# Kernel tuning notes

Measured on AMD Instinct MI355X. Metric: run time of the kernel, lower is better.

Reference implementation:

```python
import jax, jax.numpy as jnp
import numpy as np

N_NODES = 50000
N_EDGES = 600000
N_REL = 64
D = 128
N_LAYERS = 2


def setup_inputs() -> dict:
    key = jax.random.key(0)
    k1, k2, k3, k4, k5, k6 = jax.random.split(key, 6)
    return {
        "entity_table": jax.random.normal(k1, (N_NODES, D), jnp.float32) * 0.05,
        "relation_table": jax.random.normal(k2, (N_REL, D), jnp.float32) * 0.05,
        "W": jax.random.normal(k3, (N_LAYERS, 2 * D, D), jnp.float32) * 0.05,
        "b": jnp.zeros((N_LAYERS, D), jnp.float32),
        "edge_dst": jax.random.randint(k4, (N_EDGES,), 0, N_NODES),
        "edge_nbr": jax.random.randint(k5, (N_EDGES,), 0, N_NODES),
        "edge_rel": jax.random.randint(k6, (N_EDGES,), 0, N_REL),
    }


def _segment_softmax(score, seg, num_segments):
    # numerically stable per-destination-node softmax over incoming edges
    smax = jax.ops.segment_max(score, seg, num_segments=num_segments)
    ex = jnp.exp(score - smax[seg])
    denom = jax.ops.segment_sum(ex, seg, num_segments=num_segments)
    return ex / denom[seg]


def reference(entity_table, relation_table, W, b, edge_dst, edge_nbr, edge_rel):
    n_nodes, d = entity_table.shape
    n_layers = W.shape[0]
    deg = jax.ops.segment_sum(jnp.ones_like(edge_dst, dtype=entity_table.dtype),
                              edge_dst, num_segments=n_nodes)
    has_nbr = (deg > 0)[:, None]  # [N,1]

    # relation-attentive query uses the BASE entity embedding of the dst node
    # (the torch code passes entity_embedder(current_node) each layer)
    q = jnp.tanh(entity_table[edge_dst] + relation_table[edge_rel])  # [E,d]

    prev = entity_table
    for l in range(n_layers):
        nbr_emb = prev[edge_nbr]                      # [E,d] gather
        score = jnp.sum(nbr_emb * q, axis=-1)         # [E]
        alpha = _segment_softmax(score, edge_dst, n_nodes)
        neigh = jax.ops.segment_sum(alpha[:, None] * nbr_emb, edge_dst,
                                    num_segments=n_nodes)  # [N,d]
        h = jnp.concatenate([prev, neigh], axis=-1) @ W[l] + b[l]
        h = jax.nn.leaky_relu(h)                      # LeakyReLU slope 0.01
        h = h / jnp.linalg.norm(h, axis=-1, keepdims=True)
        # nodes with no neighbours keep their base entity embedding
        prev = jnp.where(has_nbr, h, entity_table)
    return prev
```

## Files before the change

kernel.cpp:

```cpp
#include <hip/hip_runtime.h>
#include <math.h>

#define NN 50000
#define NE 600000
#define NR 64
#define DD 128
#define FB 586
#define DEGS 16

typedef __attribute__((ext_vector_type(2))) _Float16 h2;
typedef __attribute__((ext_vector_type(4))) _Float16 h4;
typedef __attribute__((ext_vector_type(8))) _Float16 h8;
typedef __attribute__((ext_vector_type(4))) float f32x4;


__device__ __forceinline__ h2 tanh_h2(h2 x) {
    const h2 C5 = {(_Float16)0.1333333333f,  (_Float16)0.1333333333f};
    const h2 C3 = {(_Float16)-0.3333333333f, (_Float16)-0.3333333333f};
    const h2 ONE = {(_Float16)1.f, (_Float16)1.f};
    h2 x2 = x * x;
    h2 p = x2 * C5 + C3;
    p = x2 * p + ONE;
    return x * p;
}

template <int CTRL, int ROW_MASK>
__device__ __forceinline__ float dpp_add(float x) {
    int xi = __builtin_bit_cast(int, x);
    int yi = __builtin_amdgcn_update_dpp(0, xi, CTRL, ROW_MASK, 0xF, true);
    return x + __builtin_bit_cast(float, yi);
}


__global__ __launch_bounds__(256) void prep_k(const float* __restrict__ ent,
                                              const float* __restrict__ rel,
                                              const float* __restrict__ W,
                                              const int* __restrict__ edst,
                                              const int* __restrict__ enbr,
                                              const int* __restrict__ erel,
                                              _Float16* __restrict__ Ah,
                                              _Float16* __restrict__ relh,
                                              _Float16* __restrict__ wp,
                                              int* __restrict__ deg,
                                              int* __restrict__ bucket) {
    int b = blockIdx.x;
    if (b < FB) {
        int e = (b * 256 + threadIdx.x) * 4;
        if (e < NE) {
            int4 d  = *(const int4*)&edst[e];
            int4 nb = *(const int4*)&enbr[e];
            int4 rl = *(const int4*)&erel[e];
            int r0 = atomicAdd(&deg[d.x * DEGS], 1);
            int r1 = atomicAdd(&deg[d.y * DEGS], 1);
            int r2 = atomicAdd(&deg[d.z * DEGS], 1);
            int r3 = atomicAdd(&deg[d.w * DEGS], 1);
            if (r0 < 64) bucket[d.x * 64 + r0] = nb.x | (rl.x << 16);
            if (r1 < 64) bucket[d.y * 64 + r1] = nb.y | (rl.y << 16);
            if (r2 < 64) bucket[d.z * 64 + r2] = nb.z | (rl.z << 16);
            if (r3 < 64) bucket[d.w * 64 + r3] = nb.w | (rl.w << 16);
        }
    } else if (b < FB + 6250) {
        int tid = (b - FB) * 256 + threadIdx.x;
        int node = tid >> 5, c = tid & 31;
        float4 v = *(const float4*)&ent[(size_t)node * DD + c * 4];
        h4 o = {(_Float16)v.x, (_Float16)v.y, (_Float16)v.z, (_Float16)v.w};
        *(h4*)&Ah[(size_t)node * 256 + c * 4] = o;
    } else if (b < FB + 6258) {
        int tid = (b - FB - 6250) * 256 + threadIdx.x;
        float4 v = *(const float4*)&rel[tid * 4];
        h4 o = {(_Float16)v.x, (_Float16)v.y, (_Float16)v.z, (_Float16)v.w};
        *(h4*)&relh[tid * 4] = o;
    } else {
        int tid = (b - FB - 6258) * 256 + threadIdx.x;
        int lane = tid & 63;
        int ct   = (tid >> 6) & 7;
        int ks   = (tid >> 9) & 7;
        int l    = tid >> 12;
        int q = lane >> 4, n = lane & 15;
        const float* Wl = W + (size_t)l * 256 * 128;
        _Float16* dst = wp + ((((size_t)l * 8 + ks) * 8 + ct) * 64 + lane) * 8;
#pragma unroll
        for (int j = 0; j < 8; ++j) {
            int k = ks * 32 + q * 8 + j;
            dst[j] = (_Float16)Wl[(size_t)k * 128 + ct * 16 + n];
        }
    }
}


__global__ __launch_bounds__(256) void agg_k(const _Float16* __restrict__ Ah,
                                             const _Float16* __restrict__ Aq,
                                             const _Float16* __restrict__ relh,
                                             const int* __restrict__ deg_,
                                             const int* __restrict__ bucket,
                                             _Float16* __restrict__ Ah_out) {
    int lane = threadIdx.x & 63;
    int grp  = lane >> 4;
    int t16  = lane & 15;
    int wid  = threadIdx.x >> 6;
    int node = blockIdx.x * 4 + wid;
    int dg = deg_[node * DEGS];

    unsigned dof = (unsigned)t16 * 8u;
    h8 qv = *(const h8*)&Aq[(unsigned)node * 256u + dof];
    h2 q0 = {qv[0], qv[1]}, q1 = {qv[2], qv[3]}, q2 = {qv[4], qv[5]}, q3 = {qv[6], qv[7]};

    float l = 0.f;
    h2 acc0 = {(_Float16)0.f, (_Float16)0.f};
    h2 acc1 = acc0, acc2 = acc0, acc3 = acc0;

    if (dg > 0) {
        int e0 = node * 64;
        int e1 = e0 + dg;
        int iters = (dg + 3) >> 2;
        int last = e1 - 1;
        int ei = e0 + grp;

        int pk_c = bucket[min(ei, last)];
        h8 nb_c = *(const h8*)&Ah[(unsigned)(pk_c & 0xFFFF) * 256u + dof];
        h8 rl_c = *(const h8*)&relh[(unsigned)(pk_c >> 16) * 128u + dof];
        int pk_n = bucket[min(ei + 4, last)];

#pragma unroll 2
        for (int it = 0; it < iters; ++it) {
            int pk_n2 = bucket[min(ei + 8, last)];
            h8 nb_n = *(const h8*)&Ah[(unsigned)(pk_n & 0xFFFF) * 256u + dof];
            h8 rl_n = *(const h8*)&relh[(unsigned)(pk_n >> 16) * 128u + dof];

            h2 n0 = {nb_c[0], nb_c[1]}, n1 = {nb_c[2], nb_c[3]};
            h2 n2 = {nb_c[4], nb_c[5]}, n3 = {nb_c[6], nb_c[7]};
            h2 r0 = {rl_c[0], rl_c[1]}, r1 = {rl_c[2], rl_c[3]};
            h2 r2 = {rl_c[4], rl_c[5]}, r3 = {rl_c[6], rl_c[7]};

            h2 sd = n0 * tanh_h2(q0 + r0);
            sd = n1 * tanh_h2(q1 + r1) + sd;
            sd = n2 * tanh_h2(q2 + r2) + sd;
            sd = n3 * tanh_h2(q3 + r3) + sd;
            float s = (float)sd.x + (float)sd.y;

            s = dpp_add<0x111, 0xF>(s);
            s = dpp_add<0x112, 0xF>(s);
            s = dpp_add<0x114, 0xF>(s);
            s = dpp_add<0x118, 0xF>(s);
            int si = __builtin_amdgcn_ds_swizzle(__builtin_bit_cast(int, s), 0x1F0);
            s = __builtin_bit_cast(float, si);

            float p = (ei < e1) ? __expf(s) : 0.f;
            l += p;
            _Float16 ph = (_Float16)p;
            h2 p2 = {ph, ph};
            acc0 = p2 * n0 + acc0;
            acc1 = p2 * n1 + acc1;
            acc2 = p2 * n2 + acc2;
            acc3 = p2 * n3 + acc3;

            ei += 4;
            pk_c = pk_n; pk_n = pk_n2;
            nb_c = nb_n; rl_c = rl_n;
        }

#pragma unroll
        for (int off = 16; off <= 32; off <<= 1) {
            acc0 += __builtin_bit_cast(h2, __shfl_xor(__builtin_bit_cast(int, acc0), off, 64));
            acc1 += __builtin_bit_cast(h2, __shfl_xor(__builtin_bit_cast(int, acc1), off, 64));
            acc2 += __builtin_bit_cast(h2, __shfl_xor(__builtin_bit_cast(int, acc2), off, 64));
            acc3 += __builtin_bit_cast(h2, __shfl_xor(__builtin_bit_cast(int, acc3), off, 64));
            l += __shfl_xor(l, off, 64);
        }
    }

    float inv = (dg > 0) ? __builtin_amdgcn_rcpf(l) : 0.f;
    if (grp == 0) {
        _Float16 ih = (_Float16)inv;
        h2 iv = {ih, ih};
        h2 o0 = acc0 * iv, o1 = acc1 * iv, o2 = acc2 * iv, o3 = acc3 * iv;
        h8 o = {o0.x, o0.y, o1.x, o1.y, o2.x, o2.y, o3.x, o3.y};
        *(h8*)&Ah_out[(unsigned)node * 256u + 128u + dof] = o;
    }
}


template <bool LAST>
__global__ __launch_bounds__(256) void upd_k(const _Float16* __restrict__ Ah,
                                             const _Float16* __restrict__ wp,
                                             const float* __restrict__ bl,
                                             const int* __restrict__ deg_,
                                             const float* __restrict__ ent,
                                             float* __restrict__ out,
                                             _Float16* __restrict__ Ahn) {
    int lane = threadIdx.x & 63, wid = threadIdx.x >> 6;
    int quad = lane >> 4, n16 = lane & 15;
    int row0 = (blockIdx.x * 4 + wid) * 16;
    int arow = min(row0 + n16, NN - 1);

    f32x4 acc[8];
#pragma unroll
    for (int ct = 0; ct < 8; ++ct) acc[ct] = (f32x4){0.f, 0.f, 0.f, 0.f};

    const h8* aptr = (const h8*)(Ah + (size_t)arow * 256 + quad * 8);
#pragma unroll
    for (int ks = 0; ks < 8; ++ks) {
        h8 af = aptr[ks * 4];
        const h8* bp = (const h8*)(wp + (((size_t)ks * 8) * 64 + lane) * 8);
#pragma unroll
        for (int ct = 0; ct < 8; ++ct) {
            h8 bfrag = bp[ct * 64];
            acc[ct] = __builtin_amdgcn_mfma_f32_16x16x32_f16(af, bfrag, acc[ct], 0, 0, 0);
        }
    }

    float bias[8];
#pragma unroll
    for (int ct = 0; ct < 8; ++ct) bias[ct] = bl[ct * 16 + n16];

#pragma unroll
    for (int r = 0; r < 4; ++r) {
        int orow = row0 + quad * 4 + r;
        float h[8];
        float ss = 0.f;
#pragma unroll
        for (int ct = 0; ct < 8; ++ct) {
            float v = acc[ct][r] + bias[ct];
            v = (v > 0.f) ? v : 0.01f * v;
            h[ct] = v;
            ss += v * v;
        }
        ss = dpp_add<0x111, 0xF>(ss);
        ss = dpp_add<0x112, 0xF>(ss);
        ss = dpp_add<0x114, 0xF>(ss);
        ss = dpp_add<0x118, 0xF>(ss);
        ss = __shfl(ss, 15, 16);
        float rinv = rsqrtf(ss);

        if (orow < NN) {
            bool iso = deg_[orow * DEGS] == 0;
#pragma unroll
            for (int ct = 0; ct < 8; ++ct) {
                int col = ct * 16 + n16;
                float v = h[ct] * rinv;
                if (iso) v = ent[(size_t)orow * DD + col];
                if (LAST) out[(size_t)orow * DD + col] = v;
                else      Ahn[(size_t)orow * 256 + col] = (_Float16)v;
            }
        }
    }
}


extern "C" void kernel_launch(void* const* d_in, const int* in_sizes, int n_in,
                              void* d_out, int out_size, void* d_ws, size_t ws_size,
                              hipStream_t stream) {
    const float* ent = (const float*)d_in[0];
    const float* rel = (const float*)d_in[1];
    const float* W   = (const float*)d_in[2];
    const float* b   = (const float*)d_in[3];
    const int* edst  = (const int*)d_in[4];
    const int* enbr  = (const int*)d_in[5];
    const int* erel  = (const int*)d_in[6];
    float* out = (float*)d_out;

    char* ws = (char*)d_ws;
    size_t off = 0;
    auto alloc = [&](size_t bytes) -> void* {
        void* p = ws + off;
        off += (bytes + 255) & ~(size_t)255;
        return p;
    };
    int* deg       = (int*)alloc((size_t)NN * DEGS * 4);
    int* bucket    = (int*)alloc((size_t)NN * 64 * 4);
    _Float16* Ah0  = (_Float16*)alloc((size_t)NN * 256 * 2);
    _Float16* Ah1  = (_Float16*)alloc((size_t)NN * 256 * 2);
    _Float16* wp   = (_Float16*)alloc((size_t)2 * 8 * 8 * 64 * 8 * 2);
    _Float16* relh = (_Float16*)alloc((size_t)NR * DD * 2);

    hipMemsetAsync(deg, 0, (size_t)NN * DEGS * 4, stream);
    prep_k<<<FB + 6290, 256, 0, stream>>>(ent, rel, W, edst, enbr, erel,
                                          Ah0, relh, wp, deg, bucket);

    const _Float16* wp0 = wp;
    const _Float16* wp1 = wp + (size_t)8 * 8 * 64 * 8;
    int ublocks = (NN + 63) / 64;

    agg_k<<<NN / 4, 256, 0, stream>>>(Ah0, Ah0, relh, deg, bucket, Ah0);
    upd_k<false><<<ublocks, 256, 0, stream>>>(Ah0, wp0, b, deg, ent, out, Ah1);

    agg_k<<<NN / 4, 256, 0, stream>>>(Ah1, Ah0, relh, deg, bucket, Ah1);
    upd_k<true><<<ublocks, 256, 0, stream>>>(Ah1, wp1, b + DD, deg, ent, out, Ah0);
}
```

Measured before the change: 221.9 us.

## Compact layer-1 embedding buffer, drop gather clamps, stage update output through LDS

Layer-1 node embeddings now go into a dense 128-wide fp16 buffer instead of the first half of a 256-wide one. This halves the row stride the second aggregation gathers from and reuses Ah0's aggregation slot. The per-edge min() against the segment end is replaced by clamping the neighbour index and masking the relation id, with the bucket buffer padded so reads past the segment stay in bounds. The update kernel writes its results into a shared-memory tile and then stores whole rows with 16-byte vector writes, reading the isolated-node check once per row. The cost is extra LDS use and a __syncthreads in the update kernel.

Result: faster. 213.2 us (-3.9%).

```diff
diff --git a/kernel.cpp b/kernel.cpp
--- a/kernel.cpp
+++ b/kernel.cpp
@@ -7,6 +7,7 @@
 #define DD 128
 #define FB 586
 #define DEGS 16
+#define TS 134
 
 typedef __attribute__((ext_vector_type(2))) _Float16 h2;
 typedef __attribute__((ext_vector_type(4))) _Float16 h4;
@@ -88,12 +89,13 @@
 }
 
 
-__global__ __launch_bounds__(256) void agg_k(const _Float16* __restrict__ Ah,
+template <int NBS>
+__global__ __launch_bounds__(256) void agg_k(const _Float16* __restrict__ nbuf,
                                              const _Float16* __restrict__ Aq,
                                              const _Float16* __restrict__ relh,
                                              const int* __restrict__ deg_,
                                              const int* __restrict__ bucket,
-                                             _Float16* __restrict__ Ah_out) {
+                                             _Float16* __restrict__ aggout) {
     int lane = threadIdx.x & 63;
     int grp  = lane >> 4;
     int t16  = lane & 15;
@@ -113,19 +115,20 @@
         int e0 = node * 64;
         int e1 = e0 + dg;
         int iters = (dg + 3) >> 2;
-        int last = e1 - 1;
         int ei = e0 + grp;
 
-        int pk_c = bucket[min(ei, last)];
-        h8 nb_c = *(const h8*)&Ah[(unsigned)(pk_c & 0xFFFF) * 256u + dof];
-        h8 rl_c = *(const h8*)&relh[(unsigned)(pk_c >> 16) * 128u + dof];
-        int pk_n = bucket[min(ei + 4, last)];
+        int pk_c = bucket[ei];
+        unsigned ni_c = min((unsigned)(pk_c & 0xFFFF), (unsigned)(NN - 1));
+        h8 nb_c = *(const h8*)&nbuf[ni_c * (unsigned)NBS + dof];
+        h8 rl_c = *(const h8*)&relh[(unsigned)((pk_c >> 16) & 63) * 128u + dof];
+        int pk_n = bucket[ei + 4];
 
 #pragma unroll 2
         for (int it = 0; it < iters; ++it) {
-            int pk_n2 = bucket[min(ei + 8, last)];
-            h8 nb_n = *(const h8*)&Ah[(unsigned)(pk_n & 0xFFFF) * 256u + dof];
-            h8 rl_n = *(const h8*)&relh[(unsigned)(pk_n >> 16) * 128u + dof];
+            int pk_n2 = bucket[ei + 8];
+            unsigned ni_n = min((unsigned)(pk_n & 0xFFFF), (unsigned)(NN - 1));
+            h8 nb_n = *(const h8*)&nbuf[ni_n * (unsigned)NBS + dof];
+            h8 rl_n = *(const h8*)&relh[(unsigned)((pk_n >> 16) & 63) * 128u + dof];
 
             h2 n0 = {nb_c[0], nb_c[1]}, n1 = {nb_c[2], nb_c[3]};
             h2 n2 = {nb_c[4], nb_c[5]}, n3 = {nb_c[6], nb_c[7]};
@@ -175,19 +178,24 @@
         h2 iv = {ih, ih};
         h2 o0 = acc0 * iv, o1 = acc1 * iv, o2 = acc2 * iv, o3 = acc3 * iv;
         h8 o = {o0.x, o0.y, o1.x, o1.y, o2.x, o2.y, o3.x, o3.y};
-        *(h8*)&Ah_out[(unsigned)node * 256u + 128u + dof] = o;
-    }
-}
-
-
-template <bool LAST>
-__global__ __launch_bounds__(256) void upd_k(const _Float16* __restrict__ Ah,
+        *(h8*)&aggout[(unsigned)node * 256u + 128u + dof] = o;
+    }
+}
+
+
+template <bool LAST, int SP>
+__global__ __launch_bounds__(256) void upd_k(const _Float16* __restrict__ prev,
+                                             const _Float16* __restrict__ agg,
                                              const _Float16* __restrict__ wp,
                                              const float* __restrict__ bl,
                                              const int* __restrict__ deg_,
                                              const float* __restrict__ ent,
                                              float* __restrict__ out,
                                              _Float16* __restrict__ Ahn) {
+    __shared__ __align__(16) char ltile[64 * TS * 4];
+    float    (*t32)[TS] = (float(*)[TS])ltile;
+    _Float16 (*t16)[TS] = (_Float16(*)[TS])ltile;
+
     int lane = threadIdx.x & 63, wid = threadIdx.x >> 6;
     int quad = lane >> 4, n16 = lane & 15;
     int row0 = (blockIdx.x * 4 + wid) * 16;
@@ -197,10 +205,11 @@
 #pragma unroll
     for (int ct = 0; ct < 8; ++ct) acc[ct] = (f32x4){0.f, 0.f, 0.f, 0.f};
 
-    const h8* aptr = (const h8*)(Ah + (size_t)arow * 256 + quad * 8);
+    const h8* apP = (const h8*)(prev + (size_t)arow * SP + quad * 8);
+    const h8* apQ = (const h8*)(agg + (size_t)arow * 256 + 128 + quad * 8);
 #pragma unroll
     for (int ks = 0; ks < 8; ++ks) {
-        h8 af = aptr[ks * 4];
+        h8 af = (ks < 4) ? apP[ks * 4] : apQ[(ks - 4) * 4];
         const h8* bp = (const h8*)(wp + (((size_t)ks * 8) * 64 + lane) * 8);
 #pragma unroll
         for (int ct = 0; ct < 8; ++ct) {
@@ -215,7 +224,7 @@
 
 #pragma unroll
     for (int r = 0; r < 4; ++r) {
-        int orow = row0 + quad * 4 + r;
+        int lrow = wid * 16 + quad * 4 + r;
         float h[8];
         float ss = 0.f;
 #pragma unroll
@@ -232,15 +241,49 @@
         ss = __shfl(ss, 15, 16);
         float rinv = rsqrtf(ss);
 
-        if (orow < NN) {
-            bool iso = deg_[orow * DEGS] == 0;
-#pragma unroll
-            for (int ct = 0; ct < 8; ++ct) {
-                int col = ct * 16 + n16;
-                float v = h[ct] * rinv;
-                if (iso) v = ent[(size_t)orow * DD + col];
-                if (LAST) out[(size_t)orow * DD + col] = v;
-                else      Ahn[(size_t)orow * 256 + col] = (_Float16)v;
+#pragma unroll
+        for (int ct = 0; ct < 8; ++ct) {
+            int col = ct * 16 + n16;
+            float v = h[ct] * rinv;
+            if (LAST) t32[lrow][col] = v;
+            else      t16[lrow][col] = (_Float16)v;
+        }
+    }
+
+    __syncthreads();
+
+    int t = threadIdx.x;
+    int lrow = t >> 2, q = t & 3;
+    int grow = blockIdx.x * 64 + lrow;
+    if (grow < NN) {
+        bool iso = deg_[grow * DEGS] == 0;
+        const float* erow = ent + (size_t)grow * DD + q * 32;
+        if (!LAST) {
+            _Float16* dst = Ahn + (size_t)grow * 128 + q * 32;
+            if (!iso) {
+#pragma unroll
+                for (int k = 0; k < 4; ++k)
+                    *(h8*)&dst[k * 8] = *(const h8*)&t16[lrow][q * 32 + k * 8];
+            } else {
+#pragma unroll
+                for (int k = 0; k < 4; ++k) {
+                    float4 a = *(const float4*)&erow[k * 8];
+                    float4 c = *(const float4*)&erow[k * 8 + 4];
+                    h8 o = {(_Float16)a.x, (_Float16)a.y, (_Float16)a.z, (_Float16)a.w,
+                            (_Float16)c.x, (_Float16)c.y, (_Float16)c.z, (_Float16)c.w};
+                    *(h8*)&dst[k * 8] = o;
+                }
+            }
+        } else {
+            float* dst = out + (size_t)grow * DD + q * 32;
+            if (!iso) {
+#pragma unroll
+                for (int k = 0; k < 8; ++k)
+                    *(float4*)&dst[k * 4] = *(const float4*)&t32[lrow][q * 32 + k * 4];
+            } else {
+#pragma unroll
+                for (int k = 0; k < 8; ++k)
+                    *(float4*)&dst[k * 4] = *(const float4*)&erow[k * 4];
             }
         }
     }
@@ -267,9 +310,9 @@
         return p;
     };
     int* deg       = (int*)alloc((size_t)NN * DEGS * 4);
-    int* bucket    = (int*)alloc((size_t)NN * 64 * 4);
+    int* bucket    = (int*)alloc((size_t)NN * 64 * 4 + 256);
     _Float16* Ah0  = (_Float16*)alloc((size_t)NN * 256 * 2);
-    _Float16* Ah1  = (_Float16*)alloc((size_t)NN * 256 * 2);
+    _Float16* Ah1  = (_Float16*)alloc((size_t)NN * 128 * 2);
     _Float16* wp   = (_Float16*)alloc((size_t)2 * 8 * 8 * 64 * 8 * 2);
     _Float16* relh = (_Float16*)alloc((size_t)NR * DD * 2);
 
@@ -281,9 +324,9 @@
     const _Float16* wp1 = wp + (size_t)8 * 8 * 64 * 8;
     int ublocks = (NN + 63) / 64;
 
-    agg_k<<<NN / 4, 256, 0, stream>>>(Ah0, Ah0, relh, deg, bucket, Ah0);
-    upd_k<false><<<ublocks, 256, 0, stream>>>(Ah0, wp0, b, deg, ent, out, Ah1);
-
-    agg_k<<<NN / 4, 256, 0, stream>>>(Ah1, Ah0, relh, deg, bucket, Ah1);
-    upd_k<true><<<ublocks, 256, 0, stream>>>(Ah1, wp1, b + DD, deg, ent, out, Ah0);
-}
+    agg_k<256><<<NN / 4, 256, 0, stream>>>(Ah0, Ah0, relh, deg, bucket, Ah0);
+    upd_k<false, 256><<<ublocks, 256, 0, stream>>>(Ah0, Ah0, wp0, b, deg, ent, out, Ah1);
+
+    agg_k<128><<<NN / 4, 256, 0, stream>>>(Ah1, Ah0, relh, deg, bucket, Ah0);
+    upd_k<true, 128><<<ublocks, 256, 0, stream>>>(Ah1, Ah0, wp1, b + DD, deg, ent, out, Ah1);
+}
```
